# Kernel tuning notes

Hardware: AMD Instinct MI355X
Metric: run time of the kernel (lower is better)

Reference implementation:

```python
import jax, jax.numpy as jnp
import numpy as np

K = 256      # model / per-head dim (module uses full k per head)
H = 8        # heads
B = 4
T = 2048
EPS = 1e-5   # nn.LayerNorm default eps


def _layernorm(x, gamma, beta):
    mu = jnp.mean(x, axis=-1, keepdims=True)
    var = jnp.mean(jnp.square(x - mu), axis=-1, keepdims=True)
    return (x - mu) * jax.lax.rsqrt(var + EPS) * gamma + beta


def setup_inputs() -> dict:
    key = jax.random.key(0)
    ks = jax.random.split(key, 12)
    s = lambda fan_in: 1.0 / np.sqrt(fan_in)
    return {
        "x":  jax.random.normal(ks[0], (B, T, K), dtype=jnp.float32),
        # attention projections, stored (in, out) for x @ W
        "wq": jax.random.uniform(ks[1], (K, K * H), jnp.float32, -s(K), s(K)),
        "wk": jax.random.uniform(ks[2], (K, K * H), jnp.float32, -s(K), s(K)),
        "wv": jax.random.uniform(ks[3], (K, K * H), jnp.float32, -s(K), s(K)),
        "wu": jax.random.uniform(ks[4], (K * H, K), jnp.float32, -s(K * H), s(K * H)),
        "bu": jnp.zeros((K,), jnp.float32),
        # feed-forward
        "w1": jax.random.uniform(ks[5], (K, 4 * K), jnp.float32, -s(K), s(K)),
        "b1": jnp.zeros((4 * K,), jnp.float32),
        "w2": jax.random.uniform(ks[6], (4 * K, K), jnp.float32, -s(4 * K), s(4 * K)),
        "b2": jnp.zeros((K,), jnp.float32),
        # layernorms
        "g1": jnp.ones((K,), jnp.float32),
        "be1": jnp.zeros((K,), jnp.float32),
        "g2": jnp.ones((K,), jnp.float32),
        "be2": jnp.zeros((K,), jnp.float32),
    }


def reference(x, wq, wk, wv, wu, bu, w1, b1, w2, b2, g1, be1, g2, be2):
    b, t, k = x.shape
    h = H
    scale = k ** (-0.25)  # applied to both q and k, as in the torch code
    q = (x @ wq).reshape(b, t, h, k).transpose(0, 2, 1, 3) * scale  # bhtk
    kk = (x @ wk).reshape(b, t, h, k).transpose(0, 2, 1, 3) * scale
    v = (x @ wv).reshape(b, t, h, k).transpose(0, 2, 1, 3)
    dot = jnp.einsum("bhtk,bhsk->bhts", q, kk)
    # masked=True: upper triangle (offset=1) set to -inf -> causal
    causal = jnp.tril(jnp.ones((t, t), dtype=bool))
    dot = jnp.where(causal, dot, -jnp.inf)
    attn = jax.nn.softmax(dot, axis=-1)
    out = jnp.einsum("bhts,bhsk->bhtk", attn, v)
    out = out.transpose(0, 2, 1, 3).reshape(b, t, h * k)
    attn_out = out @ wu + bu

    x = x + attn_out                    # residual=True
    x = _layernorm(x, g1, be1)          # norm=True
    ff = jnp.maximum(x @ w1 + b1, 0.0) @ w2 + b2
    x = x + ff                          # ff + residual
    x = _layernorm(x, g2, be2)
    return x
```

## Files before the change

kernel.cpp:

```cpp
#include <hip/hip_runtime.h>
#include <hip/hip_bf16.h>

#define TT 2048
#define BB 4
#define HH 8
#define KK 256
#define MM (BB*TT)
#define NQKV 6144
#define QKS 4096

typedef __attribute__((ext_vector_type(8))) short bf16x8;
typedef __attribute__((ext_vector_type(4))) float f32x4;

__device__ __forceinline__ void gld_lds16(const void* g, void* lds) {
    __builtin_amdgcn_global_load_lds(
        (const __attribute__((address_space(1))) unsigned int*)g,
        (__attribute__((address_space(3))) unsigned int*)lds, 16, 0, 0);
}

__global__ __launch_bounds__(256) void cvt_k(const float* __restrict__ in,
                                             __hip_bfloat16* __restrict__ out, int n) {
    int i = (blockIdx.x * 256 + threadIdx.x) * 4;
    if (i + 3 < n) {
        float4 v = *(const float4*)(in + i);
        out[i + 0] = __float2bfloat16(v.x);
        out[i + 1] = __float2bfloat16(v.y);
        out[i + 2] = __float2bfloat16(v.z);
        out[i + 3] = __float2bfloat16(v.w);
    }
}

__global__ __launch_bounds__(256) void transpose_cvt(const float* __restrict__ in,
                                                     __hip_bfloat16* __restrict__ out,
                                                     int R, int C) {
    __shared__ float tile[32][33];
    int c0 = blockIdx.x * 32, r0 = blockIdx.y * 32;
    int tx = threadIdx.x & 31, ty = threadIdx.x >> 5;
    #pragma unroll
    for (int i = ty; i < 32; i += 8)
        tile[i][tx] = in[(size_t)(r0 + i) * C + c0 + tx];
    __syncthreads();
    #pragma unroll
    for (int i = ty; i < 32; i += 8)
        out[(size_t)(c0 + i) * R + r0 + tx] = __float2bfloat16(tile[tx][i]);
}

template<int EPI, int BN>
__global__ __launch_bounds__(256) void gemm_k(const __hip_bfloat16* __restrict__ A,
                                              const __hip_bfloat16* __restrict__ Bt,
                                              int M, int N, int Kd,
                                              const float* __restrict__ bias,
                                              const float* __restrict__ res,
                                              void* __restrict__ outp, float scale,
                                              __hip_bfloat16* __restrict__ vtp) {
    constexpr int NF = BN / 32;
    constexpr int BPHYS = BN / 4;
    __shared__ short sA[2][128 * 64];
    __shared__ short sB[2][BN * 64];
    int tid = threadIdx.x, lane = tid & 63, wave = tid >> 6;
    int l15 = lane & 15, g = lane >> 4;
    int m0 = blockIdx.y * 128, n0 = blockIdx.x * BN;
    int wm = (wave >> 1) * 64, wn = (wave & 1) * (BN / 2);
    f32x4 acc[4][NF] = {};
    const int NT = Kd >> 6;

    auto STAGE = [&](int kt, int buf) {
        #pragma unroll
        for (int c = 0; c < 4; ++c) {
            int L = c * 4096 + tid * 16;
            int phys = L >> 9;
            int vp = ((L >> 4) & 31) ^ phys;
            int row = (vp >> 3) * 32 + phys;
            gld_lds16(A + (size_t)(m0 + row) * Kd + kt * 64 + (vp & 7) * 8,
                      (char*)sA[buf] + L);
        }
        #pragma unroll
        for (int c = 0; c < BN / 32; ++c) {
            int L = c * 4096 + tid * 16;
            int phys = L >> 9;
            int vp = ((L >> 4) & 31) ^ phys;
            int row = (vp >> 3) * BPHYS + phys;
            gld_lds16(Bt + (size_t)(n0 + row) * Kd + kt * 64 + (vp & 7) * 8,
                      (char*)sB[buf] + L);
        }
    };

    STAGE(0, 0);
    asm volatile("s_waitcnt vmcnt(0)" ::: "memory");
    __syncthreads();
    int cur = 0;
    for (int kt = 0; kt < NT; ++kt) {
        if (kt + 1 < NT) STAGE(kt + 1, cur ^ 1);
        #pragma unroll
        for (int kk = 0; kk < 2; ++kk) {
            bf16x8 af[4], bfr[NF];
            #pragma unroll
            for (int mf = 0; mf < 4; ++mf) {
                int R = wm + mf * 16 + l15;
                int v = (((R >> 5) << 3) + (kk << 2) + g) ^ (R & 31);
                af[mf] = *(const bf16x8*)((char*)sA[cur] + ((R & 31) << 9) + (v << 4));
            }
            #pragma unroll
            for (int nf = 0; nf < NF; ++nf) {
                int R = wn + nf * 16 + l15;
                int v = ((R / BPHYS) * 8 + (kk << 2) + g) ^ (R & (BPHYS - 1));
                bfr[nf] = *(const bf16x8*)((char*)sB[cur] + ((R & (BPHYS - 1)) << 9) + (v << 4));
            }
            #pragma unroll
            for (int mf = 0; mf < 4; ++mf)
                #pragma unroll
                for (int nf = 0; nf < NF; ++nf)
                    acc[mf][nf] = __builtin_amdgcn_mfma_f32_16x16x32_bf16(af[mf], bfr[nf], acc[mf][nf], 0, 0, 0);
        }
        asm volatile("s_waitcnt vmcnt(0)" ::: "memory");
        __syncthreads();
        cur ^= 1;
    }

    #pragma unroll
    for (int mf = 0; mf < 4; ++mf) {
        int rowb = m0 + wm + mf * 16 + g * 4;
        #pragma unroll
        for (int nf = 0; nf < NF; ++nf) {
            int col = n0 + wn + nf * 16 + l15;
            if (EPI == 0) {
                if (col < 4096) {
                    #pragma unroll
                    for (int r = 0; r < 4; ++r)
                        ((__hip_bfloat16*)outp)[(size_t)(rowb + r) * QKS + col] =
                            __float2bfloat16(acc[mf][nf][r] * scale);
                } else {
                    int hv = col - 4096, h = hv >> 8, d = hv & 255;
                    int b = rowb >> 11, t = rowb & 2047;
                    ushort4 w;
                    w.x = __bfloat16_as_ushort(__float2bfloat16(acc[mf][nf][0]));
                    w.y = __bfloat16_as_ushort(__float2bfloat16(acc[mf][nf][1]));
                    w.z = __bfloat16_as_ushort(__float2bfloat16(acc[mf][nf][2]));
                    w.w = __bfloat16_as_ushort(__float2bfloat16(acc[mf][nf][3]));
                    *(ushort4*)(vtp + ((size_t)((b * 8 + h) * 256 + d)) * TT + t) = w;
                }
            } else {
                #pragma unroll
                for (int r = 0; r < 4; ++r) {
                    float v = acc[mf][nf][r];
                    size_t idx = (size_t)(rowb + r) * N + col;
                    if (EPI == 1) {
                        ((float*)outp)[idx] = v + bias[col] + res[idx];
                    } else {
                        v += bias[col];
                        ((__hip_bfloat16*)outp)[idx] = __float2bfloat16(v > 0.0f ? v : 0.0f);
                    }
                }
            }
        }
    }
}

__global__ __launch_bounds__(512, 2) void attn_k(const __hip_bfloat16* __restrict__ QK,
                                                 const __hip_bfloat16* __restrict__ VT,
                                                 __hip_bfloat16* __restrict__ O) {
    __shared__ char Kl[2][32768];
    __shared__ char Vl[2][32768];
    __shared__ char Pl[8][2048];
    int tid = threadIdx.x, lane = tid & 63, wave = tid >> 6;
    int id = blockIdx.x;
    int xcd = id & 7, w = id >> 3;
    int bh = xcd * 4 + (w >> 3);
    int jtp = w & 7;
    int b = bh >> 3, h = bh & 7;
    const __hip_bfloat16* Qb = QK + (size_t)b * TT * QKS + h * KK;
    const __hip_bfloat16* Kb = Qb + 2048;
    const __hip_bfloat16* Vtb = VT + (size_t)bh * KK * TT;

    int l15 = lane & 15, g = lane >> 4;
    int koff = g * 8;
    int koffB = g * 16;
    int pswz = (l15 & 7) << 4;

    auto STAGE = [&](int s0, int buf) {
        #pragma unroll
        for (int rd = 0; rd < 4; ++rd) {
            int L = rd * 8192 + tid * 16;
            int row = L >> 9;
            int cb = (L & 511) ^ ((row & 7) << 4);
            gld_lds16((const char*)(Kb + (size_t)(s0 + row) * QKS) + cb,
                      Kl[buf] + rd * 8192 + wave * 1024);
        }
        #pragma unroll
        for (int rd = 0; rd < 4; ++rd) {
            int L = rd * 8192 + tid * 16;
            int row = L >> 7;
            int cb = (L & 127) ^ ((row & 7) << 4);
            gld_lds16((const char*)(Vtb + (size_t)row * TT + s0) + cb,
                      Vl[buf] + rd * 8192 + wave * 1024);
        }
    };

    #pragma unroll 1
    for (int half = 0; half < 2; ++half) {
        int jt = (half == 0) ? jtp : 15 - jtp;
        int q0 = jt * 128;
        int rowbase = q0 + wave * 16;
        bf16x8 qf[8];
        #pragma unroll
        for (int kk = 0; kk < 8; ++kk)
            qf[kk] = *(const bf16x8*)(Qb + (size_t)(rowbase + l15) * QKS + kk * 32 + koff);

        f32x4 Oa[16] = {};
        float mrow = -__builtin_inff();
        float lrow = 0.f;

        STAGE(0, 0);
        asm volatile("s_waitcnt vmcnt(0)" ::: "memory");
        __syncthreads();
        int cur = 0;
        const int niter = 2 * jt + 2;

        #pragma unroll 1
        for (int i = 0; i < niter; ++i) {
            int s0 = i * 64;
            if (i + 1 < niter) STAGE(s0 + 64, cur ^ 1);

            if (s0 <= rowbase + 15) {
                f32x4 S[4] = {};
                __builtin_amdgcn_s_setprio(1);
                #pragma unroll
                for (int nf = 0; nf < 4; ++nf) {
                    int r = nf * 16 + l15;
                    int swz = (r & 7) << 4;
                    #pragma unroll
                    for (int kk = 0; kk < 8; ++kk) {
                        bf16x8 kf = *(const bf16x8*)(Kl[cur] + r * 512 + ((kk * 64 + koffB) ^ swz));
                        S[nf] = __builtin_amdgcn_mfma_f32_16x16x32_bf16(kf, qf[kk], S[nf], 0, 0, 0);
                    }
                }
                __builtin_amdgcn_s_setprio(0);
                if (s0 + 63 > rowbase) {
                    int qg = rowbase + l15;
                    #pragma unroll
                    for (int nf = 0; nf < 4; ++nf)
                        #pragma unroll
                        for (int r = 0; r < 4; ++r) {
                            int sg = s0 + nf * 16 + g * 4 + r;
                            if (sg > qg) S[nf][r] = -__builtin_inff();
                        }
                }
                float mx = S[0][0];
                #pragma unroll
                for (int nf = 0; nf < 4; ++nf)
                    #pragma unroll
                    for (int r = 0; r < 4; ++r) mx = fmaxf(mx, S[nf][r]);
                mx = fmaxf(mx, __shfl_xor(mx, 16));
                mx = fmaxf(mx, __shfl_xor(mx, 32));
                if (__any(mx > mrow + 8.0f)) {
                    float mn = fmaxf(mrow, mx);
                    float alpha = exp2f(mrow - mn);
                    mrow = mn;
                    lrow *= alpha;
                    float al[4];
                    #pragma unroll
                    for (int r = 0; r < 4; ++r) al[r] = __shfl(alpha, (g << 2) + r);
                    #pragma unroll
                    for (int nf2 = 0; nf2 < 16; ++nf2)
                        #pragma unroll
                        for (int r = 0; r < 4; ++r) Oa[nf2][r] *= al[r];
                }
                float ps = 0.f;
                #pragma unroll
                for (int nf = 0; nf < 4; ++nf)
                    #pragma unroll
                    for (int r = 0; r < 4; ++r) {
                        float p = exp2f(S[nf][r] - mrow);
                        S[nf][r] = p; ps += p;
                    }
                ps += __shfl_xor(ps, 16);
                ps += __shfl_xor(ps, 32);
                lrow += ps;
                #pragma unroll
                for (int nf = 0; nf < 4; ++nf) {
                    uint2 pk2;
                    pk2.x = (unsigned)__bfloat16_as_ushort(__float2bfloat16(S[nf][0]))
                          | ((unsigned)__bfloat16_as_ushort(__float2bfloat16(S[nf][1])) << 16);
                    pk2.y = (unsigned)__bfloat16_as_ushort(__float2bfloat16(S[nf][2]))
                          | ((unsigned)__bfloat16_as_ushort(__float2bfloat16(S[nf][3])) << 16);
                    *(uint2*)(Pl[wave] + l15 * 128 + ((nf * 32 + g * 8) ^ pswz)) = pk2;
                }
                bf16x8 pa[2];
                #pragma unroll
                for (int kk2 = 0; kk2 < 2; ++kk2)
                    pa[kk2] = *(const bf16x8*)(Pl[wave] + l15 * 128 + ((kk2 * 64 + koffB) ^ pswz));
                __builtin_amdgcn_s_setprio(1);
                #pragma unroll
                for (int nf2 = 0; nf2 < 16; ++nf2) {
                    int r = nf2 * 16 + l15;
                    int swz = (r & 7) << 4;
                    #pragma unroll
                    for (int kk2 = 0; kk2 < 2; ++kk2) {
                        bf16x8 vb = *(const bf16x8*)(Vl[cur] + r * 128 + ((kk2 * 64 + koffB) ^ swz));
                        Oa[nf2] = __builtin_amdgcn_mfma_f32_16x16x32_bf16(pa[kk2], vb, Oa[nf2], 0, 0, 0);
                    }
                }
                __builtin_amdgcn_s_setprio(0);
            }
            asm volatile("s_waitcnt vmcnt(0)" ::: "memory");
            __syncthreads();
            cur ^= 1;
        }
        float rcp_ = 1.0f / lrow;
        float rc[4];
        #pragma unroll
        for (int r = 0; r < 4; ++r) rc[r] = __shfl(rcp_, (g << 2) + r);
        #pragma unroll
        for (int nf2 = 0; nf2 < 16; ++nf2) {
            int col = nf2 * 16 + l15;
            #pragma unroll
            for (int r = 0; r < 4; ++r) {
                int t = rowbase + g * 4 + r;
                O[((size_t)b * TT + t) * 2048 + h * KK + col] = __float2bfloat16(Oa[nf2][r] * rc[r]);
            }
        }
    }
}

__global__ __launch_bounds__(256) void layernorm_k(const float* __restrict__ y,
                                                   const float* __restrict__ g,
                                                   const float* __restrict__ be,
                                                   float* __restrict__ out_f,
                                                   __hip_bfloat16* __restrict__ out_b) {
    int row = blockIdx.x * 4 + (threadIdx.x >> 6);
    int lane = threadIdx.x & 63;
    float4 v = *(const float4*)(y + (size_t)row * 256 + lane * 4);
    float s = v.x + v.y + v.z + v.w;
    #pragma unroll
    for (int d = 1; d < 64; d <<= 1) s += __shfl_xor(s, d);
    float mu = s * (1.0f / 256.0f);
    float dx = v.x - mu, dy = v.y - mu, dz = v.z - mu, dw = v.w - mu;
    float q = dx * dx + dy * dy + dz * dz + dw * dw;
    #pragma unroll
    for (int d = 1; d < 64; d <<= 1) q += __shfl_xor(q, d);
    float rs = rsqrtf(q * (1.0f / 256.0f) + 1e-5f);
    float4 gg = *(const float4*)(g + lane * 4);
    float4 bb = *(const float4*)(be + lane * 4);
    float4 o;
    o.x = dx * rs * gg.x + bb.x;
    o.y = dy * rs * gg.y + bb.y;
    o.z = dz * rs * gg.z + bb.z;
    o.w = dw * rs * gg.w + bb.w;
    *(float4*)(out_f + (size_t)row * 256 + lane * 4) = o;
    if (out_b) {
        size_t i = (size_t)row * 256 + lane * 4;
        out_b[i + 0] = __float2bfloat16(o.x);
        out_b[i + 1] = __float2bfloat16(o.y);
        out_b[i + 2] = __float2bfloat16(o.z);
        out_b[i + 3] = __float2bfloat16(o.w);
    }
}

extern "C" void kernel_launch(void* const* d_in, const int* in_sizes, int n_in,
                              void* d_out, int out_size, void* d_ws, size_t ws_size,
                              hipStream_t stream) {
    const float* x  = (const float*)d_in[0];
    const float* wq = (const float*)d_in[1];
    const float* wk = (const float*)d_in[2];
    const float* wv = (const float*)d_in[3];
    const float* wu = (const float*)d_in[4];
    const float* bu = (const float*)d_in[5];
    const float* w1 = (const float*)d_in[6];
    const float* b1 = (const float*)d_in[7];
    const float* w2 = (const float*)d_in[8];
    const float* b2 = (const float*)d_in[9];
    const float* g1 = (const float*)d_in[10];
    const float* be1 = (const float*)d_in[11];
    const float* g2 = (const float*)d_in[12];
    const float* be2 = (const float*)d_in[13];

    char* p = (char*)d_ws;
    auto alloc = [&](size_t bytes) { char* r = p; p += bytes; return r; };
    __hip_bfloat16* xb    = (__hip_bfloat16*)alloc((size_t)MM * KK * 2);
    __hip_bfloat16* wqkvT = (__hip_bfloat16*)alloc((size_t)NQKV * KK * 2);
    __hip_bfloat16* wuT   = (__hip_bfloat16*)alloc((size_t)KK * 2048 * 2);
    __hip_bfloat16* w1T   = (__hip_bfloat16*)alloc((size_t)1024 * KK * 2);
    __hip_bfloat16* w2T   = (__hip_bfloat16*)alloc((size_t)KK * 1024 * 2);
    __hip_bfloat16* qk    = (__hip_bfloat16*)alloc((size_t)MM * QKS * 2);
    __hip_bfloat16* vt    = (__hip_bfloat16*)alloc((size_t)32 * KK * TT * 2);
    __hip_bfloat16* attn  = (__hip_bfloat16*)alloc((size_t)MM * 2048 * 2);
    float*          y1    = (float*)alloc((size_t)MM * KK * 4);
    float*          x1    = (float*)alloc((size_t)MM * KK * 4);
    __hip_bfloat16* x1b   = (__hip_bfloat16*)alloc((size_t)MM * KK * 2);
    __hip_bfloat16* hid   = (__hip_bfloat16*)alloc((size_t)MM * 1024 * 2);
    float*          y2    = (float*)alloc((size_t)MM * KK * 4);

    cvt_k<<<(MM * KK) / 1024, 256, 0, stream>>>(x, xb, MM * KK);
    transpose_cvt<<<dim3(64, 8),  256, 0, stream>>>(wq, wqkvT,             256, 2048);
    transpose_cvt<<<dim3(64, 8),  256, 0, stream>>>(wk, wqkvT + 2048 * 256, 256, 2048);
    transpose_cvt<<<dim3(64, 8),  256, 0, stream>>>(wv, wqkvT + 4096 * 256, 256, 2048);
    transpose_cvt<<<dim3(8, 64),  256, 0, stream>>>(wu, wuT, 2048, 256);
    transpose_cvt<<<dim3(32, 8),  256, 0, stream>>>(w1, w1T, 256, 1024);
    transpose_cvt<<<dim3(8, 32),  256, 0, stream>>>(w2, w2T, 1024, 256);

    gemm_k<0, 128><<<dim3(NQKV / 128, MM / 128), 256, 0, stream>>>(
        xb, wqkvT, MM, NQKV, 256, nullptr, nullptr, qk, 0.3002806f, vt);

    attn_k<<<dim3(256), 512, 0, stream>>>(qk, vt, attn);

    gemm_k<1, 64><<<dim3(4, MM / 128), 256, 0, stream>>>(
        attn, wuT, MM, 256, 2048, bu, x, y1, 1.0f, nullptr);
    layernorm_k<<<MM / 4, 256, 0, stream>>>(y1, g1, be1, x1, x1b);

    gemm_k<2, 128><<<dim3(8, MM / 128), 256, 0, stream>>>(
        x1b, w1T, MM, 1024, 256, b1, nullptr, hid, 1.0f, nullptr);
    gemm_k<1, 64><<<dim3(4, MM / 128), 256, 0, stream>>>(
        hid, w2T, MM, 256, 1024, b2, x1, y2, 1.0f, nullptr);
    layernorm_k<<<MM / 4, 256, 0, stream>>>(y2, g2, be2, (float*)d_out, nullptr);
}
```

Before: 259.1 us.

## Fuse LayerNorm into full-row GEMM epilogues and merge prep kernels

The seven conversion and transpose launches are merged into one prep kernel with a block-index dispatch. The two output-projection GEMMs now use BN=256 tiles so each block owns whole 256-wide rows. Bias, residual and LayerNorm are computed in the epilogue through a cross-wave reduction in shared memory, which removes the separate layernorm kernels and the fp32 intermediate round-trips. In exchange, the grid for those GEMMs shrinks to 64 blocks, which under-fills the GPU, and LDS and register pressure rise with the larger B tile. The variance is now computed as E[x^2]-mu^2, which is less numerically robust than the two-pass form.

```diff
diff --git a/kernel.cpp b/kernel.cpp
--- a/kernel.cpp
+++ b/kernel.cpp
@@ -18,24 +18,40 @@
         (__attribute__((address_space(3))) unsigned int*)lds, 16, 0, 0);
 }
 
-__global__ __launch_bounds__(256) void cvt_k(const float* __restrict__ in,
-                                             __hip_bfloat16* __restrict__ out, int n) {
-    int i = (blockIdx.x * 256 + threadIdx.x) * 4;
-    if (i + 3 < n) {
-        float4 v = *(const float4*)(in + i);
-        out[i + 0] = __float2bfloat16(v.x);
-        out[i + 1] = __float2bfloat16(v.y);
-        out[i + 2] = __float2bfloat16(v.z);
-        out[i + 3] = __float2bfloat16(v.w);
-    }
-}
-
-__global__ __launch_bounds__(256) void transpose_cvt(const float* __restrict__ in,
-                                                     __hip_bfloat16* __restrict__ out,
-                                                     int R, int C) {
+__global__ __launch_bounds__(256) void prep_k(
+    const float* __restrict__ x, __hip_bfloat16* __restrict__ xb,
+    const float* __restrict__ wq, const float* __restrict__ wk,
+    const float* __restrict__ wv, const float* __restrict__ wu,
+    const float* __restrict__ w1, const float* __restrict__ w2,
+    __hip_bfloat16* __restrict__ wqkvT, __hip_bfloat16* __restrict__ wuT,
+    __hip_bfloat16* __restrict__ w1T, __hip_bfloat16* __restrict__ w2T) {
     __shared__ float tile[32][33];
-    int c0 = blockIdx.x * 32, r0 = blockIdx.y * 32;
-    int tx = threadIdx.x & 31, ty = threadIdx.x >> 5;
+    int bid = blockIdx.x, tid = threadIdx.x;
+    if (bid < 2048) {
+        int i = (bid * 256 + tid) * 4;
+        float4 v = *(const float4*)(x + i);
+        xb[i + 0] = __float2bfloat16(v.x);
+        xb[i + 1] = __float2bfloat16(v.y);
+        xb[i + 2] = __float2bfloat16(v.z);
+        xb[i + 3] = __float2bfloat16(v.w);
+        return;
+    }
+    int t = bid - 2048;
+    const float* in; __hip_bfloat16* out; int R, C, cx, ry;
+    if (t < 1536) {
+        int j = t >> 9, u = t & 511;
+        in = (j == 0) ? wq : (j == 1 ? wk : wv);
+        out = wqkvT + (size_t)j * 2048 * 256;
+        R = 256; C = 2048; cx = u & 63; ry = u >> 6;
+    } else if (t < 2048) {
+        int u = t - 1536; in = wu; out = wuT; R = 2048; C = 256; cx = u & 7; ry = u >> 3;
+    } else if (t < 2304) {
+        int u = t - 2048; in = w1; out = w1T; R = 256; C = 1024; cx = u & 31; ry = u >> 5;
+    } else {
+        int u = t - 2304; in = w2; out = w2T; R = 1024; C = 256; cx = u & 7; ry = u >> 3;
+    }
+    int c0 = cx * 32, r0 = ry * 32;
+    int tx = tid & 31, ty = tid >> 5;
     #pragma unroll
     for (int i = ty; i < 32; i += 8)
         tile[i][tx] = in[(size_t)(r0 + i) * C + c0 + tx];
@@ -52,11 +68,17 @@
                                               const float* __restrict__ bias,
                                               const float* __restrict__ res,
                                               void* __restrict__ outp, float scale,
-                                              __hip_bfloat16* __restrict__ vtp) {
+                                              __hip_bfloat16* __restrict__ vtp,
+                                              const float* __restrict__ gamma,
+                                              const float* __restrict__ beta,
+                                              __hip_bfloat16* __restrict__ outb) {
     constexpr int NF = BN / 32;
     constexpr int BPHYS = BN / 4;
+    constexpr int SWZM = (BPHYS - 1) & 31;
     __shared__ short sA[2][128 * 64];
     __shared__ short sB[2][BN * 64];
+    __shared__ float redS[EPI == 1 ? 128 : 1][2];
+    __shared__ float redQ[EPI == 1 ? 128 : 1][2];
     int tid = threadIdx.x, lane = tid & 63, wave = tid >> 6;
     int l15 = lane & 15, g = lane >> 4;
     int m0 = blockIdx.y * 128, n0 = blockIdx.x * BN;
@@ -78,7 +100,7 @@
         for (int c = 0; c < BN / 32; ++c) {
             int L = c * 4096 + tid * 16;
             int phys = L >> 9;
-            int vp = ((L >> 4) & 31) ^ phys;
+            int vp = ((L >> 4) & 31) ^ (phys & SWZM);
             int row = (vp >> 3) * BPHYS + phys;
             gld_lds16(Bt + (size_t)(n0 + row) * Kd + kt * 64 + (vp & 7) * 8,
                       (char*)sB[buf] + L);
@@ -103,8 +125,8 @@
             #pragma unroll
             for (int nf = 0; nf < NF; ++nf) {
                 int R = wn + nf * 16 + l15;
-                int v = ((R / BPHYS) * 8 + (kk << 2) + g) ^ (R & (BPHYS - 1));
-                bfr[nf] = *(const bf16x8*)((char*)sB[cur] + ((R & (BPHYS - 1)) << 9) + (v << 4));
+                int v = ((R / BPHYS) * 8 + (kk << 2) + g) ^ (R & SWZM);
+                bfr[nf] = *(const bf16x8*)((char*)sB[cur] + ((R % BPHYS) << 9) + (v << 4));
             }
             #pragma unroll
             for (int mf = 0; mf < 4; ++mf)
@@ -115,6 +137,50 @@
         asm volatile("s_waitcnt vmcnt(0)" ::: "memory");
         __syncthreads();
         cur ^= 1;
+    }
+
+    if (EPI == 1) {
+        #pragma unroll
+        for (int mf = 0; mf < 4; ++mf) {
+            #pragma unroll
+            for (int r = 0; r < 4; ++r) {
+                int lrow = wm + mf * 16 + g * 4 + r;
+                int rowb = m0 + lrow;
+                float s = 0.f, qq = 0.f;
+                #pragma unroll
+                for (int nf = 0; nf < NF; ++nf) {
+                    int col = n0 + wn + nf * 16 + l15;
+                    float v = acc[mf][nf][r] + bias[col] + res[(size_t)rowb * N + col];
+                    acc[mf][nf][r] = v;
+                    s += v; qq += v * v;
+                }
+                #pragma unroll
+                for (int d = 1; d < 16; d <<= 1) { s += __shfl_xor(s, d); qq += __shfl_xor(qq, d); }
+                if (l15 == 0) { redS[lrow][wave & 1] = s; redQ[lrow][wave & 1] = qq; }
+            }
+        }
+        __syncthreads();
+        #pragma unroll
+        for (int mf = 0; mf < 4; ++mf) {
+            #pragma unroll
+            for (int r = 0; r < 4; ++r) {
+                int lrow = wm + mf * 16 + g * 4 + r;
+                int rowb = m0 + lrow;
+                float s = redS[lrow][0] + redS[lrow][1];
+                float qq = redQ[lrow][0] + redQ[lrow][1];
+                float mu = s * (1.0f / 256.0f);
+                float rs = rsqrtf(qq * (1.0f / 256.0f) - mu * mu + 1e-5f);
+                #pragma unroll
+                for (int nf = 0; nf < NF; ++nf) {
+                    int col = n0 + wn + nf * 16 + l15;
+                    size_t idx = (size_t)rowb * N + col;
+                    float o = (acc[mf][nf][r] - mu) * rs * gamma[col] + beta[col];
+                    ((float*)outp)[idx] = o;
+                    if (outb) outb[idx] = __float2bfloat16(o);
+                }
+            }
+        }
+        return;
     }
 
     #pragma unroll
@@ -142,14 +208,9 @@
             } else {
                 #pragma unroll
                 for (int r = 0; r < 4; ++r) {
-                    float v = acc[mf][nf][r];
-                    size_t idx = (size_t)(rowb + r) * N + col;
-                    if (EPI == 1) {
-                        ((float*)outp)[idx] = v + bias[col] + res[idx];
-                    } else {
-                        v += bias[col];
-                        ((__hip_bfloat16*)outp)[idx] = __float2bfloat16(v > 0.0f ? v : 0.0f);
-                    }
+                    float v = acc[mf][nf][r] + bias[col];
+                    ((__hip_bfloat16*)outp)[(size_t)(rowb + r) * N + col] =
+                        __float2bfloat16(v > 0.0f ? v : 0.0f);
                 }
             }
         }
@@ -319,40 +380,6 @@
                 O[((size_t)b * TT + t) * 2048 + h * KK + col] = __float2bfloat16(Oa[nf2][r] * rc[r]);
             }
         }
-    }
-}
-
-__global__ __launch_bounds__(256) void layernorm_k(const float* __restrict__ y,
-                                                   const float* __restrict__ g,
-                                                   const float* __restrict__ be,
-                                                   float* __restrict__ out_f,
-                                                   __hip_bfloat16* __restrict__ out_b) {
-    int row = blockIdx.x * 4 + (threadIdx.x >> 6);
-    int lane = threadIdx.x & 63;
-    float4 v = *(const float4*)(y + (size_t)row * 256 + lane * 4);
-    float s = v.x + v.y + v.z + v.w;
-    #pragma unroll
-    for (int d = 1; d < 64; d <<= 1) s += __shfl_xor(s, d);
-    float mu = s * (1.0f / 256.0f);
-    float dx = v.x - mu, dy = v.y - mu, dz = v.z - mu, dw = v.w - mu;
-    float q = dx * dx + dy * dy + dz * dz + dw * dw;
-    #pragma unroll
-    for (int d = 1; d < 64; d <<= 1) q += __shfl_xor(q, d);
-    float rs = rsqrtf(q * (1.0f / 256.0f) + 1e-5f);
-    float4 gg = *(const float4*)(g + lane * 4);
-    float4 bb = *(const float4*)(be + lane * 4);
-    float4 o;
-    o.x = dx * rs * gg.x + bb.x;
-    o.y = dy * rs * gg.y + bb.y;
-    o.z = dz * rs * gg.z + bb.z;
-    o.w = dw * rs * gg.w + bb.w;
-    *(float4*)(out_f + (size_t)row * 256 + lane * 4) = o;
-    if (out_b) {
-        size_t i = (size_t)row * 256 + lane * 4;
-        out_b[i + 0] = __float2bfloat16(o.x);
-        out_b[i + 1] = __float2bfloat16(o.y);
-        out_b[i + 2] = __float2bfloat16(o.z);
-        out_b[i + 3] = __float2bfloat16(o.w);
     }
 }
 
@@ -384,32 +411,26 @@
     __hip_bfloat16* qk    = (__hip_bfloat16*)alloc((size_t)MM * QKS * 2);
     __hip_bfloat16* vt    = (__hip_bfloat16*)alloc((size_t)32 * KK * TT * 2);
     __hip_bfloat16* attn  = (__hip_bfloat16*)alloc((size_t)MM * 2048 * 2);
-    float*          y1    = (float*)alloc((size_t)MM * KK * 4);
     float*          x1    = (float*)alloc((size_t)MM * KK * 4);
     __hip_bfloat16* x1b   = (__hip_bfloat16*)alloc((size_t)MM * KK * 2);
     __hip_bfloat16* hid   = (__hip_bfloat16*)alloc((size_t)MM * 1024 * 2);
-    float*          y2    = (float*)alloc((size_t)MM * KK * 4);
-
-    cvt_k<<<(MM * KK) / 1024, 256, 0, stream>>>(x, xb, MM * KK);
-    transpose_cvt<<<dim3(64, 8),  256, 0, stream>>>(wq, wqkvT,             256, 2048);
-    transpose_cvt<<<dim3(64, 8),  256, 0, stream>>>(wk, wqkvT + 2048 * 256, 256, 2048);
-    transpose_cvt<<<dim3(64, 8),  256, 0, stream>>>(wv, wqkvT + 4096 * 256, 256, 2048);
-    transpose_cvt<<<dim3(8, 64),  256, 0, stream>>>(wu, wuT, 2048, 256);
-    transpose_cvt<<<dim3(32, 8),  256, 0, stream>>>(w1, w1T, 256, 1024);
-    transpose_cvt<<<dim3(8, 32),  256, 0, stream>>>(w2, w2T, 1024, 256);
+
+    prep_k<<<4608, 256, 0, stream>>>(x, xb, wq, wk, wv, wu, w1, w2,
+                                     wqkvT, wuT, w1T, w2T);
 
     gemm_k<0, 128><<<dim3(NQKV / 128, MM / 128), 256, 0, stream>>>(
-        xb, wqkvT, MM, NQKV, 256, nullptr, nullptr, qk, 0.3002806f, vt);
+        xb, wqkvT, MM, NQKV, 256, nullptr, nullptr, qk, 0.3002806f, vt,
+        nullptr, nullptr, nullptr);
 
     attn_k<<<dim3(256), 512, 0, stream>>>(qk, vt, attn);
 
-    gemm_k<1, 64><<<dim3(4, MM / 128), 256, 0, stream>>>(
-        attn, wuT, MM, 256, 2048, bu, x, y1, 1.0f, nullptr);
-    layernorm_k<<<MM / 4, 256, 0, stream>>>(y1, g1, be1, x1, x1b);
+    gemm_k<1, 256><<<dim3(1, MM / 128), 256, 0, stream>>>(
+        attn, wuT, MM, 256, 2048, bu, x, x1, 1.0f, nullptr, g1, be1, x1b);
 
     gemm_k<2, 128><<<dim3(8, MM / 128), 256, 0, stream>>>(
-        x1b, w1T, MM, 1024, 256, b1, nullptr, hid, 1.0f, nullptr);
-    gemm_k<1, 64><<<dim3(4, MM / 128), 256, 0, stream>>>(
-        hid, w2T, MM, 256, 1024, b2, x1, y2, 1.0f, nullptr);
-    layernorm_k<<<MM / 4, 256, 0, stream>>>(y2, g2, be2, (float*)d_out, nullptr);
+        x1b, w1T, MM, 1024, 256, b1, nullptr, hid, 1.0f, nullptr,
+        nullptr, nullptr, nullptr);
+
+    gemm_k<1, 256><<<dim3(1, MM / 128), 256, 0, stream>>>(
+        hid, w2T, MM, 256, 1024, b2, x1, (float*)d_out, 1.0f, nullptr, g2, be2, nullptr);
 }
```

New measurement: 285.5 us. +10.2%, slower.

## Fuse prep kernels and widen LDS swizzles in attention and GEMM

Applied to the files above, without the earlier changes.

Merges the x conversion and six weight transpose/convert launches into a single prep kernel dispatched by block index, removing launch overhead. It also changes the attention kernel's K tile swizzle from 8-row to 32-row XOR patterns. The V^T tile is relaid into 512-byte rows with a 32-way swizzle, aimed at cutting LDS bank conflicts on the PV MFMA operand reads. The GEMM B-tile swizzle is masked to 5 bits. The new index arithmetic adds ALU work and risks layout mismatches between the staging writes and the reads.

```diff
diff --git a/kernel.cpp b/kernel.cpp
--- a/kernel.cpp
+++ b/kernel.cpp
@@ -18,24 +18,40 @@
         (__attribute__((address_space(3))) unsigned int*)lds, 16, 0, 0);
 }
 
-__global__ __launch_bounds__(256) void cvt_k(const float* __restrict__ in,
-                                             __hip_bfloat16* __restrict__ out, int n) {
-    int i = (blockIdx.x * 256 + threadIdx.x) * 4;
-    if (i + 3 < n) {
-        float4 v = *(const float4*)(in + i);
-        out[i + 0] = __float2bfloat16(v.x);
-        out[i + 1] = __float2bfloat16(v.y);
-        out[i + 2] = __float2bfloat16(v.z);
-        out[i + 3] = __float2bfloat16(v.w);
-    }
-}
-
-__global__ __launch_bounds__(256) void transpose_cvt(const float* __restrict__ in,
-                                                     __hip_bfloat16* __restrict__ out,
-                                                     int R, int C) {
+__global__ __launch_bounds__(256) void prep_k(
+    const float* __restrict__ x, __hip_bfloat16* __restrict__ xb,
+    const float* __restrict__ wq, const float* __restrict__ wk,
+    const float* __restrict__ wv, const float* __restrict__ wu,
+    const float* __restrict__ w1, const float* __restrict__ w2,
+    __hip_bfloat16* __restrict__ wqkvT, __hip_bfloat16* __restrict__ wuT,
+    __hip_bfloat16* __restrict__ w1T, __hip_bfloat16* __restrict__ w2T) {
     __shared__ float tile[32][33];
-    int c0 = blockIdx.x * 32, r0 = blockIdx.y * 32;
-    int tx = threadIdx.x & 31, ty = threadIdx.x >> 5;
+    int bid = blockIdx.x, tid = threadIdx.x;
+    if (bid < 2048) {
+        int i = (bid * 256 + tid) * 4;
+        float4 v = *(const float4*)(x + i);
+        xb[i + 0] = __float2bfloat16(v.x);
+        xb[i + 1] = __float2bfloat16(v.y);
+        xb[i + 2] = __float2bfloat16(v.z);
+        xb[i + 3] = __float2bfloat16(v.w);
+        return;
+    }
+    int t = bid - 2048;
+    const float* in; __hip_bfloat16* out; int R, C, cx, ry;
+    if (t < 1536) {
+        int j = t >> 9, u = t & 511;
+        in = (j == 0) ? wq : (j == 1 ? wk : wv);
+        out = wqkvT + (size_t)j * 2048 * 256;
+        R = 256; C = 2048; cx = u & 63; ry = u >> 6;
+    } else if (t < 2048) {
+        int u = t - 1536; in = wu; out = wuT; R = 2048; C = 256; cx = u & 7; ry = u >> 3;
+    } else if (t < 2304) {
+        int u = t - 2048; in = w1; out = w1T; R = 256; C = 1024; cx = u & 31; ry = u >> 5;
+    } else {
+        int u = t - 2304; in = w2; out = w2T; R = 1024; C = 256; cx = u & 7; ry = u >> 3;
+    }
+    int c0 = cx * 32, r0 = ry * 32;
+    int tx = tid & 31, ty = tid >> 5;
     #pragma unroll
     for (int i = ty; i < 32; i += 8)
         tile[i][tx] = in[(size_t)(r0 + i) * C + c0 + tx];
@@ -55,6 +71,7 @@
                                               __hip_bfloat16* __restrict__ vtp) {
     constexpr int NF = BN / 32;
     constexpr int BPHYS = BN / 4;
+    constexpr int SWZM = (BPHYS - 1) & 31;
     __shared__ short sA[2][128 * 64];
     __shared__ short sB[2][BN * 64];
     int tid = threadIdx.x, lane = tid & 63, wave = tid >> 6;
@@ -78,7 +95,7 @@
         for (int c = 0; c < BN / 32; ++c) {
             int L = c * 4096 + tid * 16;
             int phys = L >> 9;
-            int vp = ((L >> 4) & 31) ^ phys;
+            int vp = ((L >> 4) & 31) ^ (phys & SWZM);
             int row = (vp >> 3) * BPHYS + phys;
             gld_lds16(Bt + (size_t)(n0 + row) * Kd + kt * 64 + (vp & 7) * 8,
                       (char*)sB[buf] + L);
@@ -103,8 +120,8 @@
             #pragma unroll
             for (int nf = 0; nf < NF; ++nf) {
                 int R = wn + nf * 16 + l15;
-                int v = ((R / BPHYS) * 8 + (kk << 2) + g) ^ (R & (BPHYS - 1));
-                bfr[nf] = *(const bf16x8*)((char*)sB[cur] + ((R & (BPHYS - 1)) << 9) + (v << 4));
+                int v = ((R / BPHYS) * 8 + (kk << 2) + g) ^ (R & SWZM);
+                bfr[nf] = *(const bf16x8*)((char*)sB[cur] + ((R % BPHYS) << 9) + (v << 4));
             }
             #pragma unroll
             for (int mf = 0; mf < 4; ++mf)
@@ -182,16 +199,18 @@
         for (int rd = 0; rd < 4; ++rd) {
             int L = rd * 8192 + tid * 16;
             int row = L >> 9;
-            int cb = (L & 511) ^ ((row & 7) << 4);
+            int cb = (L & 511) ^ ((row & 31) << 4);
             gld_lds16((const char*)(Kb + (size_t)(s0 + row) * QKS) + cb,
                       Kl[buf] + rd * 8192 + wave * 1024);
         }
         #pragma unroll
         for (int rd = 0; rd < 4; ++rd) {
             int L = rd * 8192 + tid * 16;
-            int row = L >> 7;
-            int cb = (L & 127) ^ ((row & 7) << 4);
-            gld_lds16((const char*)(Vtb + (size_t)row * TT + s0) + cb,
+            int R = L >> 9;
+            int q = (L >> 4) & 31;
+            int gl = q ^ (R & 31);
+            int d = (gl >> 3) * 64 + R;
+            gld_lds16((const char*)(Vtb + (size_t)d * TT + s0 + (gl & 7) * 8),
                       Vl[buf] + rd * 8192 + wave * 1024);
         }
     };
@@ -227,7 +246,7 @@
                 #pragma unroll
                 for (int nf = 0; nf < 4; ++nf) {
                     int r = nf * 16 + l15;
-                    int swz = (r & 7) << 4;
+                    int swz = (r & 31) << 4;
                     #pragma unroll
                     for (int kk = 0; kk < 8; ++kk) {
                         bf16x8 kf = *(const bf16x8*)(Kl[cur] + r * 512 + ((kk * 64 + koffB) ^ swz));
@@ -292,11 +311,13 @@
                 __builtin_amdgcn_s_setprio(1);
                 #pragma unroll
                 for (int nf2 = 0; nf2 < 16; ++nf2) {
-                    int r = nf2 * 16 + l15;
-                    int swz = (r & 7) << 4;
+                    int d = nf2 * 16 + l15;
+                    int R = d & 63;
                     #pragma unroll
                     for (int kk2 = 0; kk2 < 2; ++kk2) {
-                        bf16x8 vb = *(const bf16x8*)(Vl[cur] + r * 128 + ((kk2 * 64 + koffB) ^ swz));
+                        int gl = ((d >> 6) << 3) | (kk2 * 4 + g);
+                        int q = gl ^ (R & 31);
+                        bf16x8 vb = *(const bf16x8*)(Vl[cur] + R * 512 + (q << 4));
                         Oa[nf2] = __builtin_amdgcn_mfma_f32_16x16x32_bf16(pa[kk2], vb, Oa[nf2], 0, 0, 0);
                     }
                 }
@@ -390,13 +411,8 @@
     __hip_bfloat16* hid   = (__hip_bfloat16*)alloc((size_t)MM * 1024 * 2);
     float*          y2    = (float*)alloc((size_t)MM * KK * 4);
 
-    cvt_k<<<(MM * KK) / 1024, 256, 0, stream>>>(x, xb, MM * KK);
-    transpose_cvt<<<dim3(64, 8),  256, 0, stream>>>(wq, wqkvT,             256, 2048);
-    transpose_cvt<<<dim3(64, 8),  256, 0, stream>>>(wk, wqkvT + 2048 * 256, 256, 2048);
-    transpose_cvt<<<dim3(64, 8),  256, 0, stream>>>(wv, wqkvT + 4096 * 256, 256, 2048);
-    transpose_cvt<<<dim3(8, 64),  256, 0, stream>>>(wu, wuT, 2048, 256);
-    transpose_cvt<<<dim3(32, 8),  256, 0, stream>>>(w1, w1T, 256, 1024);
-    transpose_cvt<<<dim3(8, 32),  256, 0, stream>>>(w2, w2T, 1024, 256);
+    prep_k<<<4608, 256, 0, stream>>>(x, xb, wq, wk, wv, wu, w1, w2,
+                                     wqkvT, wuT, w1T, w2T);
 
     gemm_k<0, 128><<<dim3(NQKV / 128, MM / 128), 256, 0, stream>>>(
         xb, wqkvT, MM, NQKV, 256, nullptr, nullptr, qk, 0.3002806f, vt);
@@ -409,6 +425,7 @@
 
     gemm_k<2, 128><<<dim3(8, MM / 128), 256, 0, stream>>>(
         x1b, w1T, MM, 1024, 256, b1, nullptr, hid, 1.0f, nullptr);
+
     gemm_k<1, 64><<<dim3(4, MM / 128), 256, 0, stream>>>(
         hid, w2T, MM, 256, 1024, b2, x1, y2, 1.0f, nullptr);
     layernorm_k<<<MM / 4, 256, 0, stream>>>(y2, g2, be2, (float*)d_out, nullptr);
```

Result: faster. 252.7 us (-2.5%).
